# Performance work log

Hardware: AMD Instinct MI355X
Metric: run time of the kernel (lower is better)

The kernel has to match this reference:

```python
import jax, jax.numpy as jnp
import numpy as np

DIM = 1024
HEADS = 16
HEAD_DIM = DIM // HEADS
MLP_HIDDEN = int(DIM * 0.7)  # 716
EPS = 1e-5


def _ln(x, g, b):
    m = jnp.mean(x, axis=-1, keepdims=True)
    v = jnp.mean(jnp.square(x - m), axis=-1, keepdims=True)
    return (x - m) * jax.lax.rsqrt(v + EPS) * g + b


def setup_inputs() -> dict:
    key = jax.random.key(0)
    ks = jax.random.split(key, 8)
    B, N = 4, 1024
    x = jax.random.normal(ks[0], (B, N, DIM), dtype=jnp.float32)
    s = 0.02
    return {
        "x": x,
        "norm_g": jnp.ones((DIM,), jnp.float32),
        "norm_b": jnp.zeros((DIM,), jnp.float32),
        "W1": jax.random.normal(ks[1], (DIM, 3 * DIM + MLP_HIDDEN), jnp.float32) * s,
        "b1": jnp.zeros((3 * DIM + MLP_HIDDEN,), jnp.float32),
        "qn_g": jnp.ones((HEAD_DIM,), jnp.float32),
        "qn_b": jnp.zeros((HEAD_DIM,), jnp.float32),
        "kn_g": jnp.ones((HEAD_DIM,), jnp.float32),
        "kn_b": jnp.zeros((HEAD_DIM,), jnp.float32),
        "projW": jax.random.normal(ks[2], (DIM, DIM), jnp.float32) * s,
        "projb": jnp.zeros((DIM,), jnp.float32),
        "mlpW": jax.random.normal(ks[3], (MLP_HIDDEN, DIM), jnp.float32) * s,  # mlp_bias=False
        "W2": jax.random.normal(ks[4], (2 * DIM, DIM), jnp.float32) * s,
        "b2": jnp.zeros((DIM,), jnp.float32),
        "ls_g": jnp.full((DIM,), 1e-5, jnp.float32),
    }


def reference(x, norm_g, norm_b, W1, b1, qn_g, qn_b, kn_g, kn_b,
              projW, projb, mlpW, W2, b2, ls_g):
    B, N, C = x.shape
    norm_x = _ln(x, norm_g, norm_b)
    f1 = norm_x @ W1 + b1  # (B, N, 3*dim + mlp_hidden)
    qkv, mlp_hidden = f1[..., :3 * DIM], f1[..., 3 * DIM:]
    # (B, N, 3, H, hd) -> (3, B, H, N, hd)
    qkv = qkv.reshape(B, N, 3, HEADS, HEAD_DIM).transpose(2, 0, 3, 1, 4)
    q, k, v = qkv[0], qkv[1], qkv[2]
    q = _ln(q, qn_g, qn_b)
    k = _ln(k, kn_g, kn_b)
    attn = jnp.einsum('bhnd,bhmd->bhnm', q, k) * (HEAD_DIM ** -0.5)
    attn = jax.nn.softmax(attn, axis=-1)
    xo = jnp.einsum('bhnm,bhmd->bhnd', attn, v)
    xo = xo.transpose(0, 2, 1, 3).reshape(B, N, DIM)
    attn_out = xo @ projW + projb
    mlp_out = jax.nn.gelu(mlp_hidden, approximate=False) @ mlpW  # no bias
    combined = jnp.concatenate([attn_out, mlp_out], axis=-1)
    out = x + (combined @ W2 + b2) * ls_g
    return out
```

## Files before the change

### kernel.cpp

```cpp
#include <hip/hip_runtime.h>
#include <cstdint>
#include <cstddef>

typedef unsigned short u16;
typedef unsigned char u8;
typedef __attribute__((ext_vector_type(8))) u16 u16x8;
typedef __attribute__((ext_vector_type(8))) __bf16 bf16x8;
typedef __attribute__((ext_vector_type(4))) float f32x4;
typedef __attribute__((ext_vector_type(16))) float f32x16;
typedef __attribute__((ext_vector_type(4))) int i32x4;
typedef __attribute__((ext_vector_type(8))) int i32x8;
typedef __attribute__((ext_vector_type(2))) int i32x2;

__device__ __forceinline__ u16 f2bf(float f) {
  unsigned u = __builtin_bit_cast(unsigned, f);
  return (u16)((u + 0x7FFFu + ((u >> 16) & 1u)) >> 16);
}
__device__ __forceinline__ float bf2f(u16 h) {
  return __builtin_bit_cast(float, (unsigned)h << 16);
}
__device__ __forceinline__ u8 f2fp8(float f) {
  return (u8)(__builtin_amdgcn_cvt_pk_fp8_f32(f, 0.f, 0, false) & 0xFF);
}
__device__ __forceinline__ f32x16 mfma32(u16x8 a, u16x8 b, f32x16 c) {
  return __builtin_amdgcn_mfma_f32_32x32x16_bf16(
      __builtin_bit_cast(bf16x8, a), __builtin_bit_cast(bf16x8, b), c, 0, 0, 0);
}
__device__ __forceinline__ unsigned cvtpk_bf16(float lo, float hi) {
  unsigned r;
  asm("v_cvt_pk_bf16_f32 %0, %1, %2" : "=v"(r) : "v"(lo), "v"(hi));
  return r;
}
__device__ __forceinline__ float exp2_fast(float x) {
  float r;
  asm("v_exp_f32 %0, %1" : "=v"(r) : "v"(x));
  return r;
}
__device__ __forceinline__ void plswap(unsigned& a, unsigned& b) {
  i32x2 r = __builtin_amdgcn_permlane32_swap((int)a, (int)b, false, false);
  a = (unsigned)r[0];
  b = (unsigned)r[1];
}
__device__ __forceinline__ void load_lds16(const void* g, void* l) {
  __builtin_amdgcn_global_load_lds(
      (const __attribute__((address_space(1))) void*)g,
      (__attribute__((address_space(3))) void*)l, 16, 0, 0);
}

__global__ __launch_bounds__(256) void k_pre(
    const float* __restrict__ W1, const float* __restrict__ projW,
    const float* __restrict__ mlpW, const float* __restrict__ W2,
    u8* __restrict__ W1t, u8* __restrict__ pWt, u8* __restrict__ mWt,
    u8* __restrict__ W2t, const float* __restrict__ x,
    const float* __restrict__ g, const float* __restrict__ b,
    u8* __restrict__ nx8) {
  __shared__ float t[32][33];
  __shared__ float red[8];
  const int L = blockIdx.x;
  const int tid = threadIdx.x;
  if (L < 7680) {
    const float* src;
    u8* dst;
    int R, C, dR, dC, bx, by;
    if (L < 3840) {
      src = W1; dst = W1t; R = 1024; C = 3788; dR = 1024; dC = 3840;
      bx = L % 120; by = L / 120;
    } else if (L < 4864) {
      int tq = L - 3840;
      src = projW; dst = pWt; R = 1024; C = 1024; dR = 1024; dC = 1024;
      bx = tq & 31; by = tq >> 5;
    } else if (L < 5632) {
      int tq = L - 4864;
      src = mlpW; dst = mWt; R = 716; C = 1024; dR = 768; dC = 1024;
      bx = tq & 31; by = tq >> 5;
    } else {
      int tq = L - 5632;
      src = W2; dst = W2t; R = 2048; C = 1024; dR = 2048; dC = 1024;
      bx = tq & 31; by = tq >> 5;
    }
    const int n0 = bx * 32, k0 = by * 32;
    const int tx = tid & 31, ty = tid >> 5;
    const int nkt = dR >> 6;
#pragma unroll
    for (int j = 0; j < 4; ++j) {
      int kk = k0 + ty + 8 * j, nn = n0 + tx;
      float v = (kk < R && nn < C) ? src[(size_t)kk * C + nn] : 0.f;
      t[ty + 8 * j][tx] = v;
    }
    __syncthreads();
#pragma unroll
    for (int j = 0; j < 4; ++j) {
      int nn = n0 + ty + 8 * j, kk = k0 + tx;
      if (nn < dC && kk < dR) {
        const int p = nn >> 7, r = nn & 127, kt = kk >> 6, kb = kk & 63;
        dst[((size_t)(p * nkt + kt) * 128 + r) * 64 + kb] =
            f2fp8(t[tx][ty + 8 * j]);
      }
    }
  } else {
    const int row = L - 7680;
    float4 v = ((const float4*)(x + (size_t)row * 1024))[tid];
    float s = v.x + v.y + v.z + v.w;
    float ss = v.x * v.x + v.y * v.y + v.z * v.z + v.w * v.w;
#pragma unroll
    for (int off = 1; off < 64; off <<= 1) {
      s += __shfl_xor(s, off);
      ss += __shfl_xor(ss, off);
    }
    const int wid = tid >> 6, lane = tid & 63;
    if (lane == 0) { red[wid] = s; red[4 + wid] = ss; }
    __syncthreads();
    s = red[0] + red[1] + red[2] + red[3];
    ss = red[4] + red[5] + red[6] + red[7];
    const float mean = s * (1.f / 1024.f);
    const float var = ss * (1.f / 1024.f) - mean * mean;
    const float rstd = rsqrtf(var + 1e-5f);
    float4 gv = ((const float4*)g)[tid];
    float4 bv = ((const float4*)b)[tid];
    float y0 = (v.x - mean) * rstd * gv.x + bv.x;
    float y1 = (v.y - mean) * rstd * gv.y + bv.y;
    float y2 = (v.z - mean) * rstd * gv.z + bv.z;
    float y3 = (v.w - mean) * rstd * gv.w + bv.w;
    int pk = __builtin_amdgcn_cvt_pk_fp8_f32(y0, y1, 0, false);
    pk = __builtin_amdgcn_cvt_pk_fp8_f32(y2, y3, pk, true);
    ((int*)(nx8 + (size_t)row * 1024))[tid] = pk;
  }
}

__device__ __forceinline__ void gemm_fp8_core(const u8* __restrict__ A,
                                              const u8* __restrict__ B, int K,
                                              u8* Alds, u8* Blds,
                                              f32x16 (&acc)[2][2], int tid) {
  const int lane = tid & 63, wave = tid >> 6;
  const int h = lane >> 5, r32 = lane & 31;
  const int wrow = (wave >> 1) * 64, wcol = (wave & 1) * 64;
  const int srow0 = tid >> 2, spos = tid & 3;
  const int nk = K >> 6;
  auto STAGE = [&](int t, int bb) {
#pragma unroll
    for (int p = 0; p < 2; ++p) {
      const int row = p * 64 + srow0;
      const int c = spos ^ ((row >> 1) & 3);
      load_lds16(A + (size_t)row * K + (size_t)t * 64 + c * 16,
                 Alds + bb * 8192 + (p * 256 + tid) * 16);
      load_lds16(B + (size_t)t * 8192 + row * 64 + c * 16,
                 Blds + bb * 8192 + (p * 256 + tid) * 16);
    }
  };
  STAGE(0, 0);
  STAGE(1, 1);
  asm volatile("s_waitcnt vmcnt(4)" ::: "memory");
  __builtin_amdgcn_s_barrier();
  int cur = 0;
  for (int kt = 0; kt < nk; ++kt) {
    const u8* Ac = Alds + cur * 8192;
    const u8* Bc = Blds + cur * 8192;
    i32x8 af[2], bf[2];
#pragma unroll
    for (int t = 0; t < 2; ++t) {
      {
        const int row = wrow + t * 32 + r32;
        const int sw = (row >> 1) & 3;
        i32x4 lo = *(const i32x4*)(Ac + row * 64 + ((2 * h) ^ sw) * 16);
        i32x4 hi = *(const i32x4*)(Ac + row * 64 + ((2 * h + 1) ^ sw) * 16);
        i32x8 a;
        a[0] = lo[0]; a[1] = lo[1]; a[2] = lo[2]; a[3] = lo[3];
        a[4] = hi[0]; a[5] = hi[1]; a[6] = hi[2]; a[7] = hi[3];
        af[t] = a;
      }
      {
        const int row = wcol + t * 32 + r32;
        const int sw = (row >> 1) & 3;
        i32x4 lo = *(const i32x4*)(Bc + row * 64 + ((2 * h) ^ sw) * 16);
        i32x4 hi = *(const i32x4*)(Bc + row * 64 + ((2 * h + 1) ^ sw) * 16);
        i32x8 b8;
        b8[0] = lo[0]; b8[1] = lo[1]; b8[2] = lo[2]; b8[3] = lo[3];
        b8[4] = hi[0]; b8[5] = hi[1]; b8[6] = hi[2]; b8[7] = hi[3];
        bf[t] = b8;
      }
    }
    if (kt + 2 < nk) STAGE(kt + 2, cur == 0 ? 2 : cur - 1);
#pragma unroll
    for (int i = 0; i < 2; ++i)
#pragma unroll
      for (int j = 0; j < 2; ++j)
        acc[i][j] = __builtin_amdgcn_mfma_scale_f32_32x32x64_f8f6f4(
            af[i], bf[j], acc[i][j], 0, 0, 0, 0x7F7F7F7F, 0, 0x7F7F7F7F);
    if (kt + 1 < nk) {
      if (kt + 2 < nk)
        asm volatile("s_waitcnt vmcnt(4)" ::: "memory");
      else
        asm volatile("s_waitcnt vmcnt(0)" ::: "memory");
      __builtin_amdgcn_s_barrier();
    }
    cur = (cur == 2) ? 0 : cur + 1;
  }
}

__device__ __forceinline__ void gemm_fp8_core64(const u8* __restrict__ A,
                                                const u8* __restrict__ B, int K,
                                                u8* Alds, u8* Blds,
                                                f32x16 (&acc)[2], int tid) {
  const int lane = tid & 63, wave = tid >> 6;
  const int h = lane >> 5, r32 = lane & 31;
  const int wrow = (wave >> 1) * 32, wcol = (wave & 1) * 64;
  const int nk = K >> 6;
  const int ra = tid >> 2, posa = tid & 3;
  const int ca = posa ^ ((ra >> 1) & 3);
  auto STAGE = [&](int t, int bb) {
    load_lds16(A + (size_t)ra * K + (size_t)t * 64 + ca * 16,
               Alds + bb * 4096 + tid * 16);
#pragma unroll
    for (int p = 0; p < 2; ++p) {
      const int s = tid + 256 * p;
      const int r = s >> 2, pos = s & 3;
      const int c = pos ^ ((r >> 1) & 3);
      load_lds16(B + (size_t)t * 8192 + r * 64 + c * 16, Blds + bb * 8192 + s * 16);
    }
  };
  STAGE(0, 0);
  STAGE(1, 1);
  asm volatile("s_waitcnt vmcnt(3)" ::: "memory");
  __builtin_amdgcn_s_barrier();
  int cur = 0;
  for (int kt = 0; kt < nk; ++kt) {
    const u8* Ac = Alds + cur * 4096;
    const u8* Bc = Blds + cur * 8192;
    i32x8 af, bf[2];
    {
      const int row = wrow + r32;
      const int sw = (row >> 1) & 3;
      i32x4 lo = *(const i32x4*)(Ac + row * 64 + ((2 * h) ^ sw) * 16);
      i32x4 hi = *(const i32x4*)(Ac + row * 64 + ((2 * h + 1) ^ sw) * 16);
      af[0] = lo[0]; af[1] = lo[1]; af[2] = lo[2]; af[3] = lo[3];
      af[4] = hi[0]; af[5] = hi[1]; af[6] = hi[2]; af[7] = hi[3];
    }
#pragma unroll
    for (int t = 0; t < 2; ++t) {
      const int row = wcol + t * 32 + r32;
      const int sw = (row >> 1) & 3;
      i32x4 lo = *(const i32x4*)(Bc + row * 64 + ((2 * h) ^ sw) * 16);
      i32x4 hi = *(const i32x4*)(Bc + row * 64 + ((2 * h + 1) ^ sw) * 16);
      i32x8 b8;
      b8[0] = lo[0]; b8[1] = lo[1]; b8[2] = lo[2]; b8[3] = lo[3];
      b8[4] = hi[0]; b8[5] = hi[1]; b8[6] = hi[2]; b8[7] = hi[3];
      bf[t] = b8;
    }
    if (kt + 2 < nk) STAGE(kt + 2, cur == 0 ? 2 : cur - 1);
#pragma unroll
    for (int j = 0; j < 2; ++j)
      acc[j] = __builtin_amdgcn_mfma_scale_f32_32x32x64_f8f6f4(
          af, bf[j], acc[j], 0, 0, 0, 0x7F7F7F7F, 0, 0x7F7F7F7F);
    if (kt + 1 < nk) {
      if (kt + 2 < nk)
        asm volatile("s_waitcnt vmcnt(3)" ::: "memory");
      else
        asm volatile("s_waitcnt vmcnt(0)" ::: "memory");
      __builtin_amdgcn_s_barrier();
    }
    cur = (cur == 2) ? 0 : cur + 1;
  }
}

__global__ __launch_bounds__(256) void k_gemm1(
    const u8* __restrict__ nx8, const u8* __restrict__ W1t, u16* __restrict__ f1,
    const float* __restrict__ b1, const float* __restrict__ qg,
    const float* __restrict__ qb_, const float* __restrict__ kg,
    const float* __restrict__ kb_, u16* __restrict__ qbuf, u16* __restrict__ kbuf,
    u8* __restrict__ gel8) {
  __shared__ __align__(16) u8 Alds[3 * 128 * 64];
  __shared__ __align__(16) u8 Blds[3 * 128 * 64];
  const int tid = threadIdx.x;
  const int L = blockIdx.x;
  const int c = L & 7, inner = L >> 3;
  const int bm = (c & 3) * 8 + (inner & 7);
  const int bn = (c >> 2) * 15 + (inner >> 3);
  f32x16 acc[2][2];
#pragma unroll
  for (int i = 0; i < 2; ++i)
#pragma unroll
    for (int j = 0; j < 2; ++j)
#pragma unroll
      for (int r = 0; r < 16; ++r) acc[i][j][r] = 0.f;
  gemm_fp8_core(nx8 + (size_t)bm * 128 * 1024, W1t + (size_t)bn * 128 * 1024, 1024,
                Alds, Blds, acc, tid);
  const int lane = tid & 63, wave = tid >> 6;
  const int h = lane >> 5, r32 = lane & 31;
  const int wrow = (wave >> 1) * 64, wcol = (wave & 1) * 64;
  if (bn < 16) {
    const int wc = bn * 128 + wcol;
    const int which = wc >> 10;
    const int head = (wc >> 6) & 15;
    const float* g = which ? kg : qg;
    const float* bb = which ? kb_ : qb_;
    const float g0 = g[r32], g1 = g[32 + r32];
    const float be0 = bb[r32], be1 = bb[32 + r32];
    const float bias0 = b1[wc + r32], bias1 = b1[wc + 32 + r32];
    u16* dst = which ? kbuf : qbuf;
#pragma unroll
    for (int i = 0; i < 2; ++i)
#pragma unroll
      for (int r = 0; r < 16; ++r) {
        float v0 = acc[i][0][r] + bias0;
        float v1 = acc[i][1][r] + bias1;
        float s = v0 + v1, ss = v0 * v0 + v1 * v1;
#pragma unroll
        for (int off = 1; off < 32; off <<= 1) {
          s += __shfl_xor(s, off);
          ss += __shfl_xor(ss, off);
        }
        const float mean = s * (1.f / 64.f);
        const float var = ss * (1.f / 64.f) - mean * mean;
        const float rstd = rsqrtf(var + 1e-5f);
        const int row = bm * 128 + wrow + i * 32 + 4 * h + (r & 3) + 8 * (r >> 2);
        const int b = row >> 10, n = row & 1023;
        u16* orow = dst + ((size_t)(b * 16 + head) * 1024 + n) * 64;
        orow[r32] = f2bf((v0 - mean) * rstd * g0 + be0);
        orow[32 + r32] = f2bf((v1 - mean) * rstd * g1 + be1);
      }
  } else if (bn < 24) {
#pragma unroll
    for (int i = 0; i < 2; ++i)
#pragma unroll
      for (int j = 0; j < 2; ++j) {
        const int col = bn * 128 + wcol + j * 32 + r32;
        const float bs = b1[col];
#pragma unroll
        for (int r = 0; r < 16; ++r) {
          const int row = bm * 128 + wrow + i * 32 + 4 * h + (r & 3) + 8 * (r >> 2);
          f1[(size_t)row * 3840 + col] = f2bf(acc[i][j][r] + bs);
        }
      }
  } else {
#pragma unroll
    for (int i = 0; i < 2; ++i)
#pragma unroll
      for (int j = 0; j < 2; ++j) {
        const int col = bn * 128 + wcol + j * 32 + r32;
        const int cc = col - 3072;
        const bool ok = (col < 3788);
        const float bs = ok ? b1[col] : 0.f;
#pragma unroll
        for (int r = 0; r < 16; ++r) {
          const int row = bm * 128 + wrow + i * 32 + 4 * h + (r & 3) + 8 * (r >> 2);
          float y = acc[i][j][r] + bs;
          float ge = ok ? 0.5f * y * (1.f + erff(y * 0.70710678118654752f)) : 0.f;
          gel8[(size_t)row * 768 + cc] = f2fp8(ge);
        }
      }
  }
}

__global__ __launch_bounds__(256) void k_gemm_pm(
    const u8* __restrict__ xo, const u8* __restrict__ pWt,
    const u8* __restrict__ gel, const u8* __restrict__ mWt,
    u8* __restrict__ comb, const float* __restrict__ projb) {
  __shared__ __align__(16) u8 Alds[3 * 64 * 64];
  __shared__ __align__(16) u8 Blds[3 * 128 * 64];
  const int tid = threadIdx.x, bm = blockIdx.y, bnq = blockIdx.x;
  const u8* A;
  const u8* B;
  int K, colbase;
  const float* bias;
  if (bnq < 8) {
    A = xo + (size_t)bm * 64 * 1024;
    B = pWt + (size_t)bnq * 128 * 1024;
    K = 1024; colbase = bnq * 128; bias = projb;
  } else {
    A = gel + (size_t)bm * 64 * 768;
    B = mWt + (size_t)(bnq - 8) * 128 * 768;
    K = 768; colbase = 1024 + (bnq - 8) * 128; bias = nullptr;
  }
  f32x16 acc[2];
#pragma unroll
  for (int j = 0; j < 2; ++j)
#pragma unroll
    for (int r = 0; r < 16; ++r) acc[j][r] = 0.f;
  gemm_fp8_core64(A, B, K, Alds, Blds, acc, tid);
  const int lane = tid & 63, wave = tid >> 6;
  const int h = lane >> 5, r32 = lane & 31;
  const int wrow = (wave >> 1) * 32, wcol = (wave & 1) * 64;
#pragma unroll
  for (int j = 0; j < 2; ++j) {
    const int col = colbase + wcol + j * 32 + r32;
    const float bs = (bias != nullptr) ? bias[col] : 0.f;
#pragma unroll
    for (int r = 0; r < 16; ++r) {
      const int row = bm * 64 + wrow + 4 * h + (r & 3) + 8 * (r >> 2);
      comb[(size_t)row * 2048 + col] = f2fp8(acc[j][r] + bs);
    }
  }
}

__global__ __launch_bounds__(256) void k_gemm_fin(const u8* __restrict__ comb,
                                                  const u8* __restrict__ W2t,
                                                  float* __restrict__ out,
                                                  const float* __restrict__ b2,
                                                  const float* __restrict__ x,
                                                  const float* __restrict__ lsg) {
  __shared__ __align__(16) u8 Alds[3 * 64 * 64];
  __shared__ __align__(16) u8 Blds[3 * 128 * 64];
  const int tid = threadIdx.x, bm = blockIdx.y, bn = blockIdx.x;
  f32x16 acc[2];
#pragma unroll
  for (int j = 0; j < 2; ++j)
#pragma unroll
    for (int r = 0; r < 16; ++r) acc[j][r] = 0.f;
  gemm_fp8_core64(comb + (size_t)bm * 64 * 2048, W2t + (size_t)bn * 128 * 2048, 2048,
                  Alds, Blds, acc, tid);
  const int lane = tid & 63, wave = tid >> 6;
  const int h = lane >> 5, r32 = lane & 31;
  const int wrow = (wave >> 1) * 32, wcol = (wave & 1) * 64;
#pragma unroll
  for (int j = 0; j < 2; ++j) {
    const int col = bn * 128 + wcol + j * 32 + r32;
    const float bs = b2[col], ls = lsg[col];
#pragma unroll
    for (int r = 0; r < 16; ++r) {
      const int row = bm * 64 + wrow + 4 * h + (r & 3) + 8 * (r >> 2);
      out[(size_t)row * 1024 + col] =
          x[(size_t)row * 1024 + col] + (acc[j][r] + bs) * ls;
    }
  }
}

__global__ __launch_bounds__(256) void k_mid(const u16* __restrict__ f1,
                                             u16* __restrict__ vtb) {
  __shared__ u16 tt[32][33];
  const int tid = threadIdx.x;
  const int t = blockIdx.x;
  const int xq = t & 1, yq = (t >> 1) & 31, z = t >> 6;
  const int b = z >> 4, h = z & 15;
  const int d0 = xq * 32, n0 = yq * 32;
  const int tx = tid & 31, ty = tid >> 5;
#pragma unroll
  for (int j = 0; j < 4; ++j)
    tt[ty + 8 * j][tx] =
        f1[(size_t)(b * 1024 + n0 + ty + 8 * j) * 3840 + 2048 + h * 64 + d0 + tx];
  __syncthreads();
#pragma unroll
  for (int j = 0; j < 4; ++j)
    vtb[(size_t)z * 65536 + (size_t)(d0 + ty + 8 * j) * 1024 + n0 + tx] =
        tt[tx][ty + 8 * j];
}

__global__ __launch_bounds__(64) void k_flash(const u16* __restrict__ q,
                                              const u16* __restrict__ k,
                                              const u16* __restrict__ vt,
                                              u8* __restrict__ xo) {
  __shared__ __align__(16) u16 Kl[2][32 * 64];
  __shared__ __align__(16) u16 Vl[2][64 * 32];
  const int lane = threadIdx.x & 63;
  const int l31 = lane & 31, h = lane >> 5;
  const int L = blockIdx.x;
  const int xcd = L & 7, i = L >> 3;
  const int bh = xcd * 8 + (i & 7);
  const int qt = i >> 3;
  const int qrow0 = qt * 32;
  const u16* qb = q + ((size_t)bh * 1024 + qrow0) * 64;
  const u16* kb = k + (size_t)bh * 1024 * 64;
  const u16* vb = vt + (size_t)bh * 64 * 1024;

  u16x8 qf[4];
#pragma unroll
  for (int ds = 0; ds < 4; ++ds)
    qf[ds] = *(const u16x8*)(qb + (size_t)l31 * 64 + ds * 16 + h * 8);
  asm volatile("s_waitcnt vmcnt(0)" ::: "memory");

  f32x16 O[2];
#pragma unroll
  for (int d2 = 0; d2 < 2; ++d2)
#pragma unroll
    for (int r = 0; r < 16; ++r) O[d2][r] = 0.f;
  float lacc = 0.f;

  auto STAGE = [&](int t, int bb) {
#pragma unroll
    for (int p = 0; p < 4; ++p) {
      const int s = lane + 64 * p;
      const int kr = s >> 3, kslot = s & 7;
      const int kc = kslot ^ ((kr ^ (kr >> 3)) & 7);
      load_lds16(kb + (size_t)(t * 32 + kr) * 64 + kc * 8, (u16*)Kl[bb] + s * 8);
      const int vr = s >> 2, vslot = s & 3;
      const int vc = vslot ^ ((vr >> 1) & 3);
      load_lds16(vb + (size_t)vr * 1024 + t * 32 + vc * 8, (u16*)Vl[bb] + s * 8);
    }
  };
  STAGE(0, 0);
  STAGE(1, 1);

  const int swzk = (l31 & 7) ^ ((l31 >> 3) & 3);
  const float C = 0.18033688011112042f;

  f32x16 Sa, Sb;
  u16x8 vfA[4], vfB[4];

  auto READ_FRAGS = [&](int t, u16x8 (&kf)[4], u16x8 (&vf)[4]) {
    const u16* Kc = (const u16*)Kl[t & 1];
    const u16* Vc = (const u16*)Vl[t & 1];
#pragma unroll
    for (int ds = 0; ds < 4; ++ds)
      kf[ds] = *(const u16x8*)(Kc + l31 * 64 + (((ds * 2 + h) ^ swzk)) * 8);
#pragma unroll
    for (int m = 0; m < 2; ++m)
#pragma unroll
      for (int d2 = 0; d2 < 2; ++d2) {
        const int vr = d2 * 32 + l31;
        const int pos = (m * 2 + h) ^ ((vr >> 1) & 3);
        vf[m * 2 + d2] = *(const u16x8*)(Vc + vr * 32 + pos * 8);
      }
  };

  {
    asm volatile("s_waitcnt vmcnt(8)" ::: "memory");
    u16x8 kf[4];
    READ_FRAGS(0, kf, vfA);
    asm volatile("s_waitcnt lgkmcnt(0)" ::: "memory");
    __builtin_amdgcn_sched_barrier(0);
    STAGE(2, 0);
#pragma unroll
    for (int r = 0; r < 16; ++r) Sa[r] = 0.f;
    __builtin_amdgcn_s_setprio(1);
#pragma unroll
    for (int ds = 0; ds < 4; ++ds) Sa = mfma32(kf[ds], qf[ds], Sa);
    __builtin_amdgcn_s_setprio(0);
  }

  auto TILE = [&](int t, f32x16& Sc, f32x16& Sn, u16x8 (&vc)[4], u16x8 (&vn)[4]) {
    if (t < 31) {
      if (t <= 29)
        asm volatile("s_waitcnt vmcnt(8)" ::: "memory");
      else
        asm volatile("s_waitcnt vmcnt(0)" ::: "memory");
      u16x8 kf[4];
      READ_FRAGS(t + 1, kf, vn);
      asm volatile("s_waitcnt lgkmcnt(0)" ::: "memory");
      __builtin_amdgcn_sched_barrier(0);
      if (t + 3 < 32) STAGE(t + 3, (t + 3) & 1);
#pragma unroll
      for (int r = 0; r < 16; ++r) Sn[r] = 0.f;
      __builtin_amdgcn_s_setprio(1);
#pragma unroll
      for (int ds = 0; ds < 4; ++ds) Sn = mfma32(kf[ds], qf[ds], Sn);
      __builtin_amdgcn_s_setprio(0);
    }
#pragma unroll
    for (int r = 0; r < 16; ++r) {
      float pv = exp2_fast(Sc[r] * C);
      Sc[r] = pv;
      lacc += pv;
    }
    __builtin_amdgcn_s_setprio(1);
#pragma unroll
    for (int m = 0; m < 2; ++m) {
      const int ro = m * 8;
      unsigned w0 = cvtpk_bf16(Sc[ro + 0], Sc[ro + 1]);
      unsigned w2 = cvtpk_bf16(Sc[ro + 4], Sc[ro + 5]);
      unsigned w1 = cvtpk_bf16(Sc[ro + 2], Sc[ro + 3]);
      unsigned w3 = cvtpk_bf16(Sc[ro + 6], Sc[ro + 7]);
      plswap(w0, w2);
      plswap(w1, w3);
      i32x4 aw;
      aw[0] = (int)w0; aw[1] = (int)w1; aw[2] = (int)w2; aw[3] = (int)w3;
      const u16x8 pa = __builtin_bit_cast(u16x8, aw);
#pragma unroll
      for (int d2 = 0; d2 < 2; ++d2) O[d2] = mfma32(pa, vc[m * 2 + d2], O[d2]);
    }
    __builtin_amdgcn_s_setprio(0);
  };

  for (int t = 0; t < 32; t += 2) {
    TILE(t, Sa, Sb, vfA, vfB);
    TILE(t + 1, Sb, Sa, vfB, vfA);
  }

  lacc += __shfl_xor(lacc, 32);
  const float inv = 1.f / lacc;
  const int b = bh >> 4, hh = bh & 15;
#pragma unroll
  for (int r = 0; r < 16; ++r) {
    const int qr = (r & 3) + 8 * (r >> 2) + 4 * h;
    const float invr = __shfl(inv, qr);
    u8* orow = xo + (size_t)(b * 1024 + qrow0 + qr) * 1024 + hh * 64;
    orow[l31] = f2fp8(O[0][r] * invr);
    orow[32 + l31] = f2fp8(O[1][r] * invr);
  }
}

extern "C" void kernel_launch(void* const* d_in, const int* in_sizes, int n_in,
                              void* d_out, int out_size, void* d_ws, size_t ws_size,
                              hipStream_t stream) {
  (void)in_sizes; (void)n_in; (void)out_size; (void)ws_size;
  const float* x      = (const float*)d_in[0];
  const float* norm_g = (const float*)d_in[1];
  const float* norm_b = (const float*)d_in[2];
  const float* W1     = (const float*)d_in[3];
  const float* b1     = (const float*)d_in[4];
  const float* qn_g   = (const float*)d_in[5];
  const float* qn_b   = (const float*)d_in[6];
  const float* kn_g   = (const float*)d_in[7];
  const float* kn_b   = (const float*)d_in[8];
  const float* projW  = (const float*)d_in[9];
  const float* projb  = (const float*)d_in[10];
  const float* mlpW   = (const float*)d_in[11];
  const float* W2     = (const float*)d_in[12];
  const float* b2     = (const float*)d_in[13];
  const float* ls_g   = (const float*)d_in[14];

  char* ws = (char*)d_ws;
  u8*  W1t8 = (u8*)(ws + 0);
  u8*  pWt8 = (u8*)(ws + 3932160);
  u8*  mWt8 = (u8*)(ws + 4980736);
  u8*  W2t8 = (u8*)(ws + 5767168);
  u8*  nx8  = (u8*)(ws + 7864320);
  u16* f1   = (u16*)(ws + 12058624);
  u16* qbuf = (u16*)(ws + 43515904);
  u16* kbuf = (u16*)(ws + 51904512);
  u16* vtb  = (u16*)(ws + 60293120);
  u8*  gel8 = (u8*)(ws + 68681728);

  k_pre<<<11776, 256, 0, stream>>>(W1, projW, mlpW, W2, W1t8, pWt8, mWt8, W2t8,
                                   x, norm_g, norm_b, nx8);
  k_gemm1<<<960, 256, 0, stream>>>(nx8, W1t8, f1, b1, qn_g, qn_b, kn_g, kn_b,
                                   qbuf, kbuf, gel8);
  k_mid<<<4096, 256, 0, stream>>>(f1, vtb);
  k_flash<<<2048, 64, 0, stream>>>(qbuf, kbuf, vtb, nx8);
  k_gemm_pm<<<dim3(16, 64), 256, 0, stream>>>(nx8, pWt8, gel8, mWt8, (u8*)f1, projb);
  k_gemm_fin<<<dim3(8, 64), 256, 0, stream>>>((u8*)f1, W2t8, (float*)d_out, b2, x,
                                              ls_g);
}
```

Baseline: 224.3 us.

## Fuse V transpose into GEMM1 epilogue and vectorize weight FP8 packing

GEMM1 now writes the V slice of its output directly in transposed bf16 layout into the vtb buffer, which removes the separate k_mid transpose kernel and the f1 round-trip for V. The weight pre-pass switches to 64x64 tiles, packs four FP8 values per convert pair and stores 16 bytes per thread, cutting the block count and the number of scattered byte stores. The risk is that the V epilogue stores become strided across d, each writing 8 bytes per row.

After: 224.0 us. Within noise of the previous version (-0.1%).

```diff
diff --git a/kernel.cpp b/kernel.cpp
--- a/kernel.cpp
+++ b/kernel.cpp
@@ -54,51 +54,50 @@
     u8* __restrict__ W2t, const float* __restrict__ x,
     const float* __restrict__ g, const float* __restrict__ b,
     u8* __restrict__ nx8) {
-  __shared__ float t[32][33];
+  __shared__ float tt[64][65];
   __shared__ float red[8];
   const int L = blockIdx.x;
   const int tid = threadIdx.x;
-  if (L < 7680) {
+  if (L < 1920) {
     const float* src;
     u8* dst;
-    int R, C, dR, dC, bx, by;
-    if (L < 3840) {
-      src = W1; dst = W1t; R = 1024; C = 3788; dR = 1024; dC = 3840;
-      bx = L % 120; by = L / 120;
-    } else if (L < 4864) {
-      int tq = L - 3840;
-      src = projW; dst = pWt; R = 1024; C = 1024; dR = 1024; dC = 1024;
-      bx = tq & 31; by = tq >> 5;
-    } else if (L < 5632) {
-      int tq = L - 4864;
-      src = mlpW; dst = mWt; R = 716; C = 1024; dR = 768; dC = 1024;
-      bx = tq & 31; by = tq >> 5;
+    int R, C, nkt, bx, by;
+    if (L < 960) {
+      src = W1; dst = W1t; R = 1024; C = 3788; nkt = 16; bx = L / 16; by = L % 16;
+    } else if (L < 1216) {
+      int t = L - 960;
+      src = projW; dst = pWt; R = 1024; C = 1024; nkt = 16; bx = t / 16; by = t % 16;
+    } else if (L < 1408) {
+      int t = L - 1216;
+      src = mlpW; dst = mWt; R = 716; C = 1024; nkt = 12; bx = t / 12; by = t % 12;
     } else {
-      int tq = L - 5632;
-      src = W2; dst = W2t; R = 2048; C = 1024; dR = 2048; dC = 1024;
-      bx = tq & 31; by = tq >> 5;
-    }
-    const int n0 = bx * 32, k0 = by * 32;
-    const int tx = tid & 31, ty = tid >> 5;
-    const int nkt = dR >> 6;
-#pragma unroll
-    for (int j = 0; j < 4; ++j) {
-      int kk = k0 + ty + 8 * j, nn = n0 + tx;
-      float v = (kk < R && nn < C) ? src[(size_t)kk * C + nn] : 0.f;
-      t[ty + 8 * j][tx] = v;
+      int t = L - 1408;
+      src = W2; dst = W2t; R = 2048; C = 1024; nkt = 32; bx = t / 32; by = t % 32;
+    }
+    const int n0 = bx * 64, k0 = by * 64;
+    const int lr = tid >> 6, lc = tid & 63;
+#pragma unroll
+    for (int j = 0; j < 16; ++j) {
+      const int kk = k0 + lr + 4 * j, nn = n0 + lc;
+      tt[lr + 4 * j][lc] = (kk < R && nn < C) ? src[(size_t)kk * C + nn] : 0.f;
     }
     __syncthreads();
-#pragma unroll
-    for (int j = 0; j < 4; ++j) {
-      int nn = n0 + ty + 8 * j, kk = k0 + tx;
-      if (nn < dC && kk < dR) {
-        const int p = nn >> 7, r = nn & 127, kt = kk >> 6, kb = kk & 63;
-        dst[((size_t)(p * nkt + kt) * 128 + r) * 64 + kb] =
-            f2fp8(t[tx][ty + 8 * j]);
-      }
-    }
+    const int rn = tid >> 2;
+    const int kb = (tid & 3) * 16;
+    i32x4 st;
+#pragma unroll
+    for (int w = 0; w < 4; ++w) {
+      int p0 = __builtin_amdgcn_cvt_pk_fp8_f32(tt[kb + 4 * w + 0][rn],
+                                               tt[kb + 4 * w + 1][rn], 0, false);
+      p0 = __builtin_amdgcn_cvt_pk_fp8_f32(tt[kb + 4 * w + 2][rn],
+                                           tt[kb + 4 * w + 3][rn], p0, true);
+      st[w] = p0;
+    }
+    const int nn_g = n0 + rn;
+    const int p = nn_g >> 7, rr = nn_g & 127;
+    *(i32x4*)(dst + ((size_t)(p * nkt + by) * 128 + rr) * 64 + kb) = st;
   } else {
-    const int row = L - 7680;
+    const int row = L - 1920;
     float4 v = ((const float4*)(x + (size_t)row * 1024))[tid];
     float s = v.x + v.y + v.z + v.w;
     float ss = v.x * v.x + v.y * v.y + v.z * v.z + v.w * v.w;
@@ -263,11 +262,11 @@
 }
 
 __global__ __launch_bounds__(256) void k_gemm1(
-    const u8* __restrict__ nx8, const u8* __restrict__ W1t, u16* __restrict__ f1,
+    const u8* __restrict__ nx8, const u8* __restrict__ W1t,
     const float* __restrict__ b1, const float* __restrict__ qg,
     const float* __restrict__ qb_, const float* __restrict__ kg,
     const float* __restrict__ kb_, u16* __restrict__ qbuf, u16* __restrict__ kbuf,
-    u8* __restrict__ gel8) {
+    u16* __restrict__ vtb, u8* __restrict__ gel8) {
   __shared__ __align__(16) u8 Alds[3 * 128 * 64];
   __shared__ __align__(16) u8 Blds[3 * 128 * 64];
   const int tid = threadIdx.x;
@@ -324,11 +323,20 @@
 #pragma unroll
       for (int j = 0; j < 2; ++j) {
         const int col = bn * 128 + wcol + j * 32 + r32;
+        const int cv = col - 2048;
+        const int head = cv >> 6, d = cv & 63;
         const float bs = b1[col];
 #pragma unroll
-        for (int r = 0; r < 16; ++r) {
-          const int row = bm * 128 + wrow + i * 32 + 4 * h + (r & 3) + 8 * (r >> 2);
-          f1[(size_t)row * 3840 + col] = f2bf(acc[i][j][r] + bs);
+        for (int g2 = 0; g2 < 4; ++g2) {
+          const int row0 = bm * 128 + wrow + i * 32 + 4 * h + 8 * g2;
+          const int b = row0 >> 10, n = row0 & 1023;
+          ushort4 st;
+          st.x = f2bf(acc[i][j][4 * g2 + 0] + bs);
+          st.y = f2bf(acc[i][j][4 * g2 + 1] + bs);
+          st.z = f2bf(acc[i][j][4 * g2 + 2] + bs);
+          st.w = f2bf(acc[i][j][4 * g2 + 3] + bs);
+          *(ushort4*)(vtb + (size_t)(b * 16 + head) * 65536 + (size_t)d * 1024 +
+                      n) = st;
         }
       }
   } else {
@@ -424,26 +432,6 @@
   }
 }
 
-__global__ __launch_bounds__(256) void k_mid(const u16* __restrict__ f1,
-                                             u16* __restrict__ vtb) {
-  __shared__ u16 tt[32][33];
-  const int tid = threadIdx.x;
-  const int t = blockIdx.x;
-  const int xq = t & 1, yq = (t >> 1) & 31, z = t >> 6;
-  const int b = z >> 4, h = z & 15;
-  const int d0 = xq * 32, n0 = yq * 32;
-  const int tx = tid & 31, ty = tid >> 5;
-#pragma unroll
-  for (int j = 0; j < 4; ++j)
-    tt[ty + 8 * j][tx] =
-        f1[(size_t)(b * 1024 + n0 + ty + 8 * j) * 3840 + 2048 + h * 64 + d0 + tx];
-  __syncthreads();
-#pragma unroll
-  for (int j = 0; j < 4; ++j)
-    vtb[(size_t)z * 65536 + (size_t)(d0 + ty + 8 * j) * 1024 + n0 + tx] =
-        tt[tx][ty + 8 * j];
-}
-
 __global__ __launch_bounds__(64) void k_flash(const u16* __restrict__ q,
                                               const u16* __restrict__ k,
                                               const u16* __restrict__ vt,
@@ -619,11 +607,10 @@
   u16* vtb  = (u16*)(ws + 60293120);
   u8*  gel8 = (u8*)(ws + 68681728);
 
-  k_pre<<<11776, 256, 0, stream>>>(W1, projW, mlpW, W2, W1t8, pWt8, mWt8, W2t8,
-                                   x, norm_g, norm_b, nx8);
-  k_gemm1<<<960, 256, 0, stream>>>(nx8, W1t8, f1, b1, qn_g, qn_b, kn_g, kn_b,
-                                   qbuf, kbuf, gel8);
-  k_mid<<<4096, 256, 0, stream>>>(f1, vtb);
+  k_pre<<<6016, 256, 0, stream>>>(W1, projW, mlpW, W2, W1t8, pWt8, mWt8, W2t8,
+                                  x, norm_g, norm_b, nx8);
+  k_gemm1<<<960, 256, 0, stream>>>(nx8, W1t8, b1, qn_g, qn_b, kn_g, kn_b,
+                                   qbuf, kbuf, vtb, gel8);
   k_flash<<<2048, 64, 0, stream>>>(qbuf, kbuf, vtb, nx8);
   k_gemm_pm<<<dim3(16, 64), 256, 0, stream>>>(nx8, pWt8, gel8, mWt8, (u8*)f1, projb);
   k_gemm_fin<<<dim3(8, 64), 256, 0, stream>>>((u8*)f1, W2t8, (float*)d_out, b2, x,
```
